# Kernel optimization log

Hardware: AMD Instinct MI355X
Metric: run time of the kernel (lower is better)

The kernel has to match this reference:

```python
import jax, jax.numpy as jnp
import numpy as np


def setup_inputs() -> dict:
    key = jax.random.key(0)
    k1, k2 = jax.random.split(key)
    N, M, D = 16384, 4096, 512
    input = jax.random.normal(k1, (N, D), dtype=jnp.float32)
    centres = jax.random.normal(k2, (M, D), dtype=jnp.float32)
    return {"input": input, "centres": centres}


def reference(input, centres):
    # Mathematically identical to (x - c).pow(2).sum(-1) without the
    # O(N*M*D) expanded intermediate.
    x_sq = jnp.sum(input * input, axis=-1, keepdims=True)        # [N, 1]
    c_sq = jnp.sum(centres * centres, axis=-1)[None, :]          # [1, M]
    cross = jnp.einsum("nd,md->nm", input, centres)             # [N, M]
    return x_sq + c_sq - 2.0 * cross                             # [N, M]
```

## Files before the change

kernel.cpp:

```cpp
#include <hip/hip_runtime.h>
#include <hip/hip_bf16.h>
#include <stdint.h>

#define N_ROWS 16384
#define M_ROWS 4096
#define DDIM   512
#define BK     32
#define NKT    (DDIM / BK)

using frag_ab = __attribute__((ext_vector_type(8))) short;
using frag_cd = __attribute__((ext_vector_type(4))) float;

__device__ __forceinline__ unsigned short f2bf(float f) {
  unsigned int u = __float_as_uint(f);
  u += 0x7fffu + ((u >> 16) & 1u);
  return (unsigned short)(u >> 16);
}

__global__ void rbf_convert_kernel(const float* __restrict__ in,
                                   const float* __restrict__ cen,
                                   unsigned short* __restrict__ a_bf,
                                   unsigned short* __restrict__ b_bf,
                                   float* __restrict__ x_sq,
                                   float* __restrict__ c_sq) {
  const int wave = threadIdx.x >> 6;
  const int lane = threadIdx.x & 63;
  const int row  = blockIdx.x * 4 + wave;

  const float* src;
  unsigned short* dst;
  float* nrm;
  if (row < N_ROWS) {
    src = in + (long)row * DDIM;
    dst = a_bf + (long)row * DDIM;
    nrm = x_sq + row;
  } else {
    const int rr = row - N_ROWS;
    src = cen + (long)rr * DDIM;
    dst = b_bf + (long)rr * DDIM;
    nrm = c_sq + rr;
  }

  float sum = 0.f;
#pragma unroll
  for (int it = 0; it < 2; ++it) {
    const int col = it * 256 + lane * 4;
    float4 v = *(const float4*)(src + col);
    sum += v.x * v.x + v.y * v.y + v.z * v.z + v.w * v.w;
    ushort4 p;
    p.x = f2bf(v.x); p.y = f2bf(v.y); p.z = f2bf(v.z); p.w = f2bf(v.w);
    *(ushort4*)(dst + col) = p;
  }
#pragma unroll
  for (int off = 32; off > 0; off >>= 1) sum += __shfl_down(sum, off, 64);
  if (lane == 0) *nrm = sum;
}

__global__ __launch_bounds__(512, 2) void rbf_gemm_kernel(
    const unsigned short* __restrict__ a_bf,
    const unsigned short* __restrict__ b_bf,
    const float* __restrict__ x_sq,
    const float* __restrict__ c_sq,
    float* __restrict__ out) {
  __shared__ __attribute__((aligned(16))) unsigned short A_lds[4][256 * BK];
  __shared__ __attribute__((aligned(16))) unsigned short B_lds[4][256 * BK];

  const int tid    = threadIdx.x;
  const int wid    = tid >> 6;
  const int lane   = tid & 63;
  const int lane15 = lane & 15;
  const int quad   = lane >> 4;
  const int wm     = wid >> 2;
  const int wn     = wid & 3;

  const int orig = blockIdx.x;
  const int xcd  = orig & 7;
  const int s    = orig >> 3;
  const int m0   = (s >> 3) * 256;
  const int n0   = (xcd * 8 + (s & 7)) * 256;

  const unsigned short* srcA[2];
  const unsigned short* srcB[2];
  int dstc[2];
#pragma unroll
  for (int it = 0; it < 2; ++it) {
    const int o   = (it * 512 + tid) * 16;
    const int op  = o ^ ((o >> 3) & 48);
    const int row = op >> 6;
    const int ke  = (op & 63) >> 1;
    srcA[it] = a_bf + (size_t)(n0 + row) * DDIM + ke;
    srcB[it] = b_bf + (size_t)(m0 + row) * DDIM + ke;
    dstc[it] = (it * 512 + tid) * 8;
  }

  int offA[8], offB[4];
#pragma unroll
  for (int i = 0; i < 8; ++i) {
    const int row = wm * 128 + i * 16 + lane15;
    const int L   = row * 64 + quad * 16;
    offA[i] = L ^ ((L >> 3) & 48);
  }
#pragma unroll
  for (int j = 0; j < 4; ++j) {
    const int row = wn * 64 + j * 16 + lane15;
    const int L   = row * 64 + quad * 16;
    offB[j] = L ^ ((L >> 3) & 48);
  }

  frag_cd acc[8][4];
#pragma unroll
  for (int i = 0; i < 8; ++i)
#pragma unroll
    for (int j = 0; j < 4; ++j)
      acc[i][j] = (frag_cd){0.f, 0.f, 0.f, 0.f};

  auto stage = [&](int slot, int kt) {
#pragma unroll
    for (int it = 0; it < 2; ++it) {
      __builtin_amdgcn_global_load_lds(
          (const __attribute__((address_space(1))) unsigned int*)(srcA[it] + kt * BK),
          (__attribute__((address_space(3))) unsigned int*)&A_lds[slot][dstc[it]],
          16, 0, 0);
      __builtin_amdgcn_global_load_lds(
          (const __attribute__((address_space(1))) unsigned int*)(srcB[it] + kt * BK),
          (__attribute__((address_space(3))) unsigned int*)&B_lds[slot][dstc[it]],
          16, 0, 0);
    }
  };

  stage(0, 0);
  stage(1, 1);
  stage(2, 2);

#pragma unroll
  for (int kt = 0; kt < NKT; ++kt) {
    if (kt <= NKT - 3)      asm volatile("s_waitcnt vmcnt(8)" ::: "memory");
    else if (kt == NKT - 2) asm volatile("s_waitcnt vmcnt(4)" ::: "memory");
    else                    asm volatile("s_waitcnt vmcnt(0)" ::: "memory");
    __builtin_amdgcn_s_barrier();
    __builtin_amdgcn_sched_barrier(0);

    if (kt + 3 < NKT) stage((kt + 3) & 3, kt + 3);

    const char* Ab = (const char*)&A_lds[kt & 3][0];
    const char* Bb = (const char*)&B_lds[kt & 3][0];
    frag_ab a[8], b[4];
#pragma unroll
    for (int j = 0; j < 4; ++j) b[j] = *(const frag_ab*)(Bb + offB[j]);
#pragma unroll
    for (int i = 0; i < 8; ++i) a[i] = *(const frag_ab*)(Ab + offA[i]);

    __builtin_amdgcn_s_setprio(1);
#pragma unroll
    for (int i = 0; i < 8; ++i)
#pragma unroll
      for (int j = 0; j < 4; ++j)
        acc[i][j] = __builtin_amdgcn_mfma_f32_16x16x32_bf16(
            a[i], b[j], acc[i][j], 0, 0, 0);
    __builtin_amdgcn_s_setprio(0);
  }

  float cs[4];
#pragma unroll
  for (int j = 0; j < 4; ++j) cs[j] = c_sq[m0 + wn * 64 + j * 16 + lane15];

#pragma unroll
  for (int i = 0; i < 8; ++i) {
#pragma unroll
    for (int reg = 0; reg < 4; ++reg) {
      const int r = n0 + wm * 128 + i * 16 + quad * 4 + reg;
      const float xv = x_sq[r];
      float* orow = out + (size_t)r * M_ROWS + m0 + wn * 64 + lane15;
#pragma unroll
      for (int j = 0; j < 4; ++j) {
        orow[j * 16] = xv + cs[j] - 2.0f * acc[i][j][reg];
      }
    }
  }
}

extern "C" void kernel_launch(void* const* d_in, const int* in_sizes, int n_in,
                              void* d_out, int out_size, void* d_ws, size_t ws_size,
                              hipStream_t stream) {
  const float* input   = (const float*)d_in[0];
  const float* centres = (const float*)d_in[1];
  float* out = (float*)d_out;

  char* ws = (char*)d_ws;
  unsigned short* a_bf = (unsigned short*)ws;
  unsigned short* b_bf = (unsigned short*)(ws + (size_t)N_ROWS * DDIM * 2);
  float* x_sq = (float*)(ws + (size_t)N_ROWS * DDIM * 2 + (size_t)M_ROWS * DDIM * 2);
  float* c_sq = x_sq + N_ROWS;

  rbf_convert_kernel<<<(N_ROWS + M_ROWS) / 4, 256, 0, stream>>>(
      input, centres, a_bf, b_bf, x_sq, c_sq);

  rbf_gemm_kernel<<<(N_ROWS / 256) * (M_ROWS / 256), 512, 0, stream>>>(
      a_bf, b_bf, x_sq, c_sq, out);
}
```

Baseline: 356.6 us.

## Fuse bf16 conversion and norm computation into GEMM kernel

Removes the separate conversion kernel. The GEMM now loads fp32 tiles into registers, converts them to bf16, writes them to swizzled LDS and accumulates the row norms in-kernel, with register-prefetch double buffering replacing the 4-stage async global_load_lds pipeline. The block-to-tile mapping is also changed for L2 locality. This avoids the extra launch and the bf16 workspace round-trip, but each block re-reads and re-converts fp32 inputs, doubling load bytes and adding VALU work inside the main loop.

Measured after the change: 922.6 us. 2.59x slower.

```diff
diff --git a/kernel.cpp b/kernel.cpp
--- a/kernel.cpp
+++ b/kernel.cpp
@@ -17,53 +17,14 @@
   return (unsigned short)(u >> 16);
 }
 
-__global__ void rbf_convert_kernel(const float* __restrict__ in,
-                                   const float* __restrict__ cen,
-                                   unsigned short* __restrict__ a_bf,
-                                   unsigned short* __restrict__ b_bf,
-                                   float* __restrict__ x_sq,
-                                   float* __restrict__ c_sq) {
-  const int wave = threadIdx.x >> 6;
-  const int lane = threadIdx.x & 63;
-  const int row  = blockIdx.x * 4 + wave;
-
-  const float* src;
-  unsigned short* dst;
-  float* nrm;
-  if (row < N_ROWS) {
-    src = in + (long)row * DDIM;
-    dst = a_bf + (long)row * DDIM;
-    nrm = x_sq + row;
-  } else {
-    const int rr = row - N_ROWS;
-    src = cen + (long)rr * DDIM;
-    dst = b_bf + (long)rr * DDIM;
-    nrm = c_sq + rr;
-  }
-
-  float sum = 0.f;
-#pragma unroll
-  for (int it = 0; it < 2; ++it) {
-    const int col = it * 256 + lane * 4;
-    float4 v = *(const float4*)(src + col);
-    sum += v.x * v.x + v.y * v.y + v.z * v.z + v.w * v.w;
-    ushort4 p;
-    p.x = f2bf(v.x); p.y = f2bf(v.y); p.z = f2bf(v.z); p.w = f2bf(v.w);
-    *(ushort4*)(dst + col) = p;
-  }
-#pragma unroll
-  for (int off = 32; off > 0; off >>= 1) sum += __shfl_down(sum, off, 64);
-  if (lane == 0) *nrm = sum;
-}
-
-__global__ __launch_bounds__(512, 2) void rbf_gemm_kernel(
-    const unsigned short* __restrict__ a_bf,
-    const unsigned short* __restrict__ b_bf,
-    const float* __restrict__ x_sq,
-    const float* __restrict__ c_sq,
+__global__ __launch_bounds__(512, 2) void rbf_fused_kernel(
+    const float* __restrict__ in,
+    const float* __restrict__ cen,
     float* __restrict__ out) {
-  __shared__ __attribute__((aligned(16))) unsigned short A_lds[4][256 * BK];
-  __shared__ __attribute__((aligned(16))) unsigned short B_lds[4][256 * BK];
+  __shared__ __attribute__((aligned(16))) unsigned short A_lds[2][256 * BK];
+  __shared__ __attribute__((aligned(16))) unsigned short B_lds[2][256 * BK];
+  __shared__ float An[256];
+  __shared__ float Bn[256];
 
   const int tid    = threadIdx.x;
   const int wid    = tid >> 6;
@@ -76,22 +37,20 @@
   const int orig = blockIdx.x;
   const int xcd  = orig & 7;
   const int s    = orig >> 3;
-  const int m0   = (s >> 3) * 256;
-  const int n0   = (xcd * 8 + (s & 7)) * 256;
+  const int band = s >> 6;
+  const int r    = s & 63;
+  const int m0   = (r >> 2) * 256;
+  const int n0   = (band * 32 + xcd * 4 + (r & 3)) * 256;
 
-  const unsigned short* srcA[2];
-  const unsigned short* srcB[2];
-  int dstc[2];
-#pragma unroll
-  for (int it = 0; it < 2; ++it) {
-    const int o   = (it * 512 + tid) * 16;
-    const int op  = o ^ ((o >> 3) & 48);
-    const int row = op >> 6;
-    const int ke  = (op & 63) >> 1;
-    srcA[it] = a_bf + (size_t)(n0 + row) * DDIM + ke;
-    srcB[it] = b_bf + (size_t)(m0 + row) * DDIM + ke;
-    dstc[it] = (it * 512 + tid) * 8;
-  }
+  const int srow  = tid >> 1;
+  const int shalf = tid & 1;
+  const float* gA = in  + (size_t)(n0 + srow) * DDIM + shalf * 16;
+  const float* gB = cen + (size_t)(m0 + srow) * DDIM + shalf * 16;
+
+  const int Lw  = srow * 64 + shalf * 32;
+  const int sw0 = Lw ^ ((Lw >> 3) & 48);
+  const int Lw1 = Lw + 16;
+  const int sw1 = Lw1 ^ ((Lw1 >> 3) & 48);
 
   int offA[8], offB[4];
 #pragma unroll
@@ -114,36 +73,48 @@
     for (int j = 0; j < 4; ++j)
       acc[i][j] = (frag_cd){0.f, 0.f, 0.f, 0.f};
 
-  auto stage = [&](int slot, int kt) {
+  float4 ra[4], rb[4];
+  float pnA = 0.f, pnB = 0.f;
+
+  auto load_regs = [&](int kt) {
 #pragma unroll
-    for (int it = 0; it < 2; ++it) {
-      __builtin_amdgcn_global_load_lds(
-          (const __attribute__((address_space(1))) unsigned int*)(srcA[it] + kt * BK),
-          (__attribute__((address_space(3))) unsigned int*)&A_lds[slot][dstc[it]],
-          16, 0, 0);
-      __builtin_amdgcn_global_load_lds(
-          (const __attribute__((address_space(1))) unsigned int*)(srcB[it] + kt * BK),
-          (__attribute__((address_space(3))) unsigned int*)&B_lds[slot][dstc[it]],
-          16, 0, 0);
+    for (int c = 0; c < 4; ++c) {
+      ra[c] = *(const float4*)(gA + kt * BK + c * 4);
+      rb[c] = *(const float4*)(gB + kt * BK + c * 4);
     }
   };
 
-  stage(0, 0);
-  stage(1, 1);
-  stage(2, 2);
+  auto cvt_write = [&](int slot) {
+    unsigned int ua[8], ub[8];
+#pragma unroll
+    for (int c = 0; c < 4; ++c) {
+      pnA += ra[c].x * ra[c].x + ra[c].y * ra[c].y +
+             ra[c].z * ra[c].z + ra[c].w * ra[c].w;
+      pnB += rb[c].x * rb[c].x + rb[c].y * rb[c].y +
+             rb[c].z * rb[c].z + rb[c].w * rb[c].w;
+      ua[c * 2]     = (unsigned)f2bf(ra[c].x) | ((unsigned)f2bf(ra[c].y) << 16);
+      ua[c * 2 + 1] = (unsigned)f2bf(ra[c].z) | ((unsigned)f2bf(ra[c].w) << 16);
+      ub[c * 2]     = (unsigned)f2bf(rb[c].x) | ((unsigned)f2bf(rb[c].y) << 16);
+      ub[c * 2 + 1] = (unsigned)f2bf(rb[c].z) | ((unsigned)f2bf(rb[c].w) << 16);
+    }
+    char* Ab = (char*)&A_lds[slot][0];
+    char* Bb = (char*)&B_lds[slot][0];
+    *(uint4*)(Ab + sw0) = (uint4){ua[0], ua[1], ua[2], ua[3]};
+    *(uint4*)(Ab + sw1) = (uint4){ua[4], ua[5], ua[6], ua[7]};
+    *(uint4*)(Bb + sw0) = (uint4){ub[0], ub[1], ub[2], ub[3]};
+    *(uint4*)(Bb + sw1) = (uint4){ub[4], ub[5], ub[6], ub[7]};
+  };
+
+  load_regs(0);
+  cvt_write(0);
+  __syncthreads();
 
 #pragma unroll
   for (int kt = 0; kt < NKT; ++kt) {
-    if (kt <= NKT - 3)      asm volatile("s_waitcnt vmcnt(8)" ::: "memory");
-    else if (kt == NKT - 2) asm volatile("s_waitcnt vmcnt(4)" ::: "memory");
-    else                    asm volatile("s_waitcnt vmcnt(0)" ::: "memory");
-    __builtin_amdgcn_s_barrier();
-    __builtin_amdgcn_sched_barrier(0);
+    if (kt + 1 < NKT) load_regs(kt + 1);
 
-    if (kt + 3 < NKT) stage((kt + 3) & 3, kt + 3);
-
-    const char* Ab = (const char*)&A_lds[kt & 3][0];
-    const char* Bb = (const char*)&B_lds[kt & 3][0];
+    const char* Ab = (const char*)&A_lds[kt & 1][0];
+    const char* Bb = (const char*)&B_lds[kt & 1][0];
     frag_ab a[8], b[4];
 #pragma unroll
     for (int j = 0; j < 4; ++j) b[j] = *(const frag_ab*)(Bb + offB[j]);
@@ -158,19 +129,27 @@
         acc[i][j] = __builtin_amdgcn_mfma_f32_16x16x32_bf16(
             a[i], b[j], acc[i][j], 0, 0, 0);
     __builtin_amdgcn_s_setprio(0);
+
+    if (kt + 1 < NKT) cvt_write((kt + 1) & 1);
+    __syncthreads();
   }
+
+  pnA += __shfl_xor(pnA, 1, 64);
+  pnB += __shfl_xor(pnB, 1, 64);
+  if (shalf == 0) { An[srow] = pnA; Bn[srow] = pnB; }
+  __syncthreads();
 
   float cs[4];
 #pragma unroll
-  for (int j = 0; j < 4; ++j) cs[j] = c_sq[m0 + wn * 64 + j * 16 + lane15];
+  for (int j = 0; j < 4; ++j) cs[j] = Bn[wn * 64 + j * 16 + lane15];
 
 #pragma unroll
   for (int i = 0; i < 8; ++i) {
 #pragma unroll
     for (int reg = 0; reg < 4; ++reg) {
-      const int r = n0 + wm * 128 + i * 16 + quad * 4 + reg;
-      const float xv = x_sq[r];
-      float* orow = out + (size_t)r * M_ROWS + m0 + wn * 64 + lane15;
+      const int rl = wm * 128 + i * 16 + quad * 4 + reg;
+      const float xv = An[rl];
+      float* orow = out + (size_t)(n0 + rl) * M_ROWS + m0 + wn * 64 + lane15;
 #pragma unroll
       for (int j = 0; j < 4; ++j) {
         orow[j * 16] = xv + cs[j] - 2.0f * acc[i][j][reg];
@@ -186,15 +165,6 @@
   const float* centres = (const float*)d_in[1];
   float* out = (float*)d_out;
 
-  char* ws = (char*)d_ws;
-  unsigned short* a_bf = (unsigned short*)ws;
-  unsigned short* b_bf = (unsigned short*)(ws + (size_t)N_ROWS * DDIM * 2);
-  float* x_sq = (float*)(ws + (size_t)N_ROWS * DDIM * 2 + (size_t)M_ROWS * DDIM * 2);
-  float* c_sq = x_sq + N_ROWS;
-
-  rbf_convert_kernel<<<(N_ROWS + M_ROWS) / 4, 256, 0, stream>>>(
-      input, centres, a_bf, b_bf, x_sq, c_sq);
-
-  rbf_gemm_kernel<<<(N_ROWS / 256) * (M_ROWS / 256), 512, 0, stream>>>(
-      a_bf, b_bf, x_sq, c_sq, out);
+  rbf_fused_kernel<<<(N_ROWS / 256) * (M_ROWS / 256), 512, 0, stream>>>(
+      input, centres, out);
 }
```
